# Optimization experiments

Measured on AMD Instinct MI355X. Metric: run time of the kernel, lower is better.

The kernel has to match this reference:

```python
import jax, jax.numpy as jnp
import numpy as np

ALPHA = 0.2  # LeakyReLU negative slope


def setup_inputs() -> dict:
    key = jax.random.key(0)
    k0, k1, k2, k3 = jax.random.split(key, 4)
    N, E, C_IN, H, C_PH = 50000, 800000, 128, 4, 32  # per-head dim = out_channels // num_heads
    node_feats = jax.random.normal(k0, (N, C_IN), dtype=jnp.float32)
    edge_index = jax.random.randint(k1, (2, E), 0, N, dtype=jnp.int64)
    # Linear(in_channels, num_heads * per_head): W is [H*C_PH, C_IN], b is [H*C_PH]
    W = jax.random.normal(k2, (H * C_PH, C_IN), dtype=jnp.float32) * 0.1
    b = jnp.zeros((H * C_PH,), dtype=jnp.float32)
    # attention vector a: [H, 2*C_PH]
    a = jax.random.normal(k3, (H, 2 * C_PH), dtype=jnp.float32) * 0.1
    return {"node_feats": node_feats, "edge_index": edge_index, "W": W, "b": b, "a": a}


def reference(node_feats, edge_index, W, b, a):
    H, twoC = a.shape
    C = twoC // 2
    N = node_feats.shape[0]
    # Linear projection, then split heads: [N, H, C]
    h = (node_feats @ W.T + b).reshape(N, H, C)
    # logits[e,h] = <h[src_e] ++ h[dst_e], a[h]> ; split the dot product so we
    # compute per-node partial scores once and gather scalars per edge.
    s_src = jnp.einsum('nhc,hc->nh', h, a[:, :C])   # [N, H]
    s_dst = jnp.einsum('nhc,hc->nh', h, a[:, C:])   # [N, H]
    logits = s_src[edge_index[0]] + s_dst[edge_index[1]]  # [E, H]
    logits = jax.nn.leaky_relu(logits, negative_slope=ALPHA)
    # Original applies softmax over dim=-2, i.e. across ALL edges per head.
    return jax.nn.softmax(logits, axis=0)
```

## Files before the change

### kernel.cpp

```cpp
#include <hip/hip_runtime.h>

#define ALPHA 0.2f

#define WS_BIAS 1024
#define WS_SUM  1032
#define WS_S    1040

__global__ void k_init(const float* __restrict__ W, const float* __restrict__ b,
                       const float* __restrict__ a, float* __restrict__ ws) {
    int t = threadIdx.x;
    #pragma unroll
    for (int h = 0; h < 4; ++h) {
        float accS = 0.f, accD = 0.f;
        #pragma unroll
        for (int c = 0; c < 32; ++c) {
            float wv = W[(h * 32 + c) * 128 + t];
            accS = fmaf(wv, a[h * 64 + c], accS);
            accD = fmaf(wv, a[h * 64 + 32 + c], accD);
        }
        ws[h * 128 + t] = accS;
        ws[512 + h * 128 + t] = accD;
    }
    if (t < 4) {
        float bs = 0.f, bd = 0.f;
        for (int c = 0; c < 32; ++c) {
            bs = fmaf(b[t * 32 + c], a[t * 64 + c], bs);
            bd = fmaf(b[t * 32 + c], a[t * 64 + 32 + c], bd);
        }
        ws[WS_BIAS + t] = bs;
        ws[WS_BIAS + 4 + t] = bd;
        ws[WS_SUM + t] = 0.f;
    }
}

__global__ __launch_bounds__(256) void k_proj(const float* __restrict__ x,
                                              float* __restrict__ ws, int N) {
    __shared__ float lw[1152];
    __shared__ float lb[8];
    int t = threadIdx.x;
    for (int idx = t; idx < 1024; idx += 256) {
        int k = idx & 127;
        int h = (idx >> 7) & 3;
        int base = (idx < 512) ? 0 : 576;
        lw[base + h * 144 + k + 4 * (k >> 5)] = ws[idx];
    }
    if (t < 8) lb[t] = ws[WS_BIAS + t];
    __syncthreads();

    int q = t & 3;
    int node = blockIdx.x * 64 + (t >> 2);
    float aS0=0,aS1=0,aS2=0,aS3=0,aD0=0,aD1=0,aD2=0,aD3=0;
    if (node < N) {
        const float4* xp = (const float4*)(x + (size_t)node * 128 + q * 32);
        int wb = q * 36;
        #pragma unroll
        for (int i = 0; i < 8; ++i) {
            float4 xv = xp[i];
            int o = wb + i * 4;
            float4 w;
            w = *(const float4*)&lw[o];          aS0 += xv.x*w.x + xv.y*w.y + xv.z*w.z + xv.w*w.w;
            w = *(const float4*)&lw[144 + o];    aS1 += xv.x*w.x + xv.y*w.y + xv.z*w.z + xv.w*w.w;
            w = *(const float4*)&lw[288 + o];    aS2 += xv.x*w.x + xv.y*w.y + xv.z*w.z + xv.w*w.w;
            w = *(const float4*)&lw[432 + o];    aS3 += xv.x*w.x + xv.y*w.y + xv.z*w.z + xv.w*w.w;
            w = *(const float4*)&lw[576 + o];    aD0 += xv.x*w.x + xv.y*w.y + xv.z*w.z + xv.w*w.w;
            w = *(const float4*)&lw[720 + o];    aD1 += xv.x*w.x + xv.y*w.y + xv.z*w.z + xv.w*w.w;
            w = *(const float4*)&lw[864 + o];    aD2 += xv.x*w.x + xv.y*w.y + xv.z*w.z + xv.w*w.w;
            w = *(const float4*)&lw[1008 + o];   aD3 += xv.x*w.x + xv.y*w.y + xv.z*w.z + xv.w*w.w;
        }
    }
    aS0 += __shfl_xor(aS0, 1); aS0 += __shfl_xor(aS0, 2);
    aS1 += __shfl_xor(aS1, 1); aS1 += __shfl_xor(aS1, 2);
    aS2 += __shfl_xor(aS2, 1); aS2 += __shfl_xor(aS2, 2);
    aS3 += __shfl_xor(aS3, 1); aS3 += __shfl_xor(aS3, 2);
    aD0 += __shfl_xor(aD0, 1); aD0 += __shfl_xor(aD0, 2);
    aD1 += __shfl_xor(aD1, 1); aD1 += __shfl_xor(aD1, 2);
    aD2 += __shfl_xor(aD2, 1); aD2 += __shfl_xor(aD2, 2);
    aD3 += __shfl_xor(aD3, 1); aD3 += __shfl_xor(aD3, 2);
    if (q == 0 && node < N) {
        float4* sp = (float4*)(ws + WS_S + (size_t)node * 8);
        sp[0] = make_float4(aS0 + lb[0], aS1 + lb[1], aS2 + lb[2], aS3 + lb[3]);
        sp[1] = make_float4(aD0 + lb[4], aD1 + lb[5], aD2 + lb[6], aD3 + lb[7]);
    }
}

__global__ __launch_bounds__(256) void k_edge(const int* __restrict__ ei,
                                              const float* __restrict__ s,
                                              float* __restrict__ out,
                                              float* __restrict__ sums, int E) {
    int tid = blockIdx.x * blockDim.x + threadIdx.x;
    int T = gridDim.x * blockDim.x;
    float l0 = 0.f, l1 = 0.f, l2 = 0.f, l3 = 0.f;
    for (int e = tid; e < E; e += T) {
        int src = ei[e];
        int dst = ei[E + e];
        float4 ss = *(const float4*)(s + (size_t)src * 8);
        float4 sd = *(const float4*)(s + (size_t)dst * 8 + 4);
        float z0 = ss.x + sd.x, z1 = ss.y + sd.y, z2 = ss.z + sd.z, z3 = ss.w + sd.w;
        z0 = (z0 >= 0.f) ? z0 : ALPHA * z0;
        z1 = (z1 >= 0.f) ? z1 : ALPHA * z1;
        z2 = (z2 >= 0.f) ? z2 : ALPHA * z2;
        z3 = (z3 >= 0.f) ? z3 : ALPHA * z3;
        float e0 = expf(z0), e1 = expf(z1), e2 = expf(z2), e3 = expf(z3);
        *(float4*)(out + (size_t)e * 4) = make_float4(e0, e1, e2, e3);
        l0 += e0; l1 += e1; l2 += e2; l3 += e3;
    }
    #pragma unroll
    for (int m = 1; m < 64; m <<= 1) {
        l0 += __shfl_xor(l0, m);
        l1 += __shfl_xor(l1, m);
        l2 += __shfl_xor(l2, m);
        l3 += __shfl_xor(l3, m);
    }
    __shared__ float red[4][4];
    int wv = threadIdx.x >> 6;
    if ((threadIdx.x & 63) == 0) {
        red[wv][0] = l0; red[wv][1] = l1; red[wv][2] = l2; red[wv][3] = l3;
    }
    __syncthreads();
    if (threadIdx.x < 4) {
        int h = threadIdx.x;
        atomicAdd(&sums[h], red[0][h] + red[1][h] + red[2][h] + red[3][h]);
    }
}

__global__ __launch_bounds__(256) void k_scale(float* __restrict__ out,
                                               const float* __restrict__ sums, int E) {
    __shared__ float inv[4];
    if (threadIdx.x < 4) inv[threadIdx.x] = 1.0f / sums[threadIdx.x];
    __syncthreads();
    int e = blockIdx.x * blockDim.x + threadIdx.x;
    if (e < E) {
        float4 v = *(const float4*)(out + (size_t)e * 4);
        v.x *= inv[0]; v.y *= inv[1]; v.z *= inv[2]; v.w *= inv[3];
        *(float4*)(out + (size_t)e * 4) = v;
    }
}

extern "C" void kernel_launch(void* const* d_in, const int* in_sizes, int n_in,
                              void* d_out, int out_size, void* d_ws, size_t ws_size,
                              hipStream_t stream) {
    const float* x  = (const float*)d_in[0];
    const int*   ei = (const int*)d_in[1];
    const float* W  = (const float*)d_in[2];
    const float* b  = (const float*)d_in[3];
    const float* a  = (const float*)d_in[4];
    float* out = (float*)d_out;
    float* ws  = (float*)d_ws;

    const int CIN = 128;
    int N = in_sizes[0] / CIN;
    int E = in_sizes[1] / 2;

    k_init<<<1, 128, 0, stream>>>(W, b, a, ws);
    k_proj<<<(N + 63) / 64, 256, 0, stream>>>(x, ws, N);
    k_edge<<<1024, 256, 0, stream>>>(ei, ws + WS_S, out, ws + WS_SUM, E);
    k_scale<<<(E + 255) / 256, 256, 0, stream>>>(out, ws + WS_SUM, E);
}
```

Measured before the change: 119.5 us.

## Fuse weight folding into projection and recompute edge exps instead of storing

```diff
diff --git a/kernel.cpp b/kernel.cpp
--- a/kernel.cpp
+++ b/kernel.cpp
@@ -2,49 +2,40 @@
 
 #define ALPHA 0.2f
 
-#define WS_BIAS 1024
-#define WS_SUM  1032
-#define WS_S    1040
-
-__global__ void k_init(const float* __restrict__ W, const float* __restrict__ b,
-                       const float* __restrict__ a, float* __restrict__ ws) {
-    int t = threadIdx.x;
-    #pragma unroll
-    for (int h = 0; h < 4; ++h) {
-        float accS = 0.f, accD = 0.f;
-        #pragma unroll
-        for (int c = 0; c < 32; ++c) {
-            float wv = W[(h * 32 + c) * 128 + t];
-            accS = fmaf(wv, a[h * 64 + c], accS);
-            accD = fmaf(wv, a[h * 64 + 32 + c], accD);
-        }
-        ws[h * 128 + t] = accS;
-        ws[512 + h * 128 + t] = accD;
-    }
-    if (t < 4) {
-        float bs = 0.f, bd = 0.f;
-        for (int c = 0; c < 32; ++c) {
-            bs = fmaf(b[t * 32 + c], a[t * 64 + c], bs);
-            bd = fmaf(b[t * 32 + c], a[t * 64 + 32 + c], bd);
-        }
-        ws[WS_BIAS + t] = bs;
-        ws[WS_BIAS + 4 + t] = bd;
-        ws[WS_SUM + t] = 0.f;
-    }
-}
+#define WS_SUM 0
+#define WS_S   64
 
 __global__ __launch_bounds__(256) void k_proj(const float* __restrict__ x,
+                                              const float* __restrict__ W,
+                                              const float* __restrict__ b,
+                                              const float* __restrict__ a,
                                               float* __restrict__ ws, int N) {
     __shared__ float lw[1152];
     __shared__ float lb[8];
     int t = threadIdx.x;
-    for (int idx = t; idx < 1024; idx += 256) {
+    #pragma unroll
+    for (int j = 0; j < 4; ++j) {
+        int idx = t + 256 * j;
         int k = idx & 127;
         int h = (idx >> 7) & 3;
-        int base = (idx < 512) ? 0 : 576;
-        lw[base + h * 144 + k + 4 * (k >> 5)] = ws[idx];
+        int dstf = idx >> 9;
+        const float* Wp = W + (size_t)(h * 32) * 128 + k;
+        const float* ap = a + h * 64 + dstf * 32;
+        float acc = 0.f;
+        #pragma unroll
+        for (int c = 0; c < 32; ++c)
+            acc = fmaf(Wp[(size_t)c * 128], ap[c], acc);
+        lw[dstf * 576 + h * 144 + k + 4 * (k >> 5)] = acc;
     }
-    if (t < 8) lb[t] = ws[WS_BIAS + t];
+    if (t < 8) {
+        int h = t & 3, dstf = t >> 2;
+        float acc = 0.f;
+        #pragma unroll
+        for (int c = 0; c < 32; ++c)
+            acc = fmaf(b[h * 32 + c], a[h * 64 + dstf * 32 + c], acc);
+        lb[t] = acc;
+    }
+    if (blockIdx.x == 0 && t < 4) ws[WS_SUM + t * 16] = 0.f;
     __syncthreads();
 
     int q = t & 3;
@@ -83,10 +74,14 @@
     }
 }
 
-__global__ __launch_bounds__(256) void k_edge(const int* __restrict__ ei,
-                                              const float* __restrict__ s,
-                                              float* __restrict__ out,
-                                              float* __restrict__ sums, int E) {
+__device__ __forceinline__ float leaky_exp(float z) {
+    z = (z >= 0.f) ? z : ALPHA * z;
+    return __expf(z);
+}
+
+__global__ __launch_bounds__(256) void k_edge_sum(const int* __restrict__ ei,
+                                                  const float* __restrict__ s,
+                                                  float* __restrict__ sums, int E) {
     int tid = blockIdx.x * blockDim.x + threadIdx.x;
     int T = gridDim.x * blockDim.x;
     float l0 = 0.f, l1 = 0.f, l2 = 0.f, l3 = 0.f;
@@ -95,14 +90,10 @@
         int dst = ei[E + e];
         float4 ss = *(const float4*)(s + (size_t)src * 8);
         float4 sd = *(const float4*)(s + (size_t)dst * 8 + 4);
-        float z0 = ss.x + sd.x, z1 = ss.y + sd.y, z2 = ss.z + sd.z, z3 = ss.w + sd.w;
-        z0 = (z0 >= 0.f) ? z0 : ALPHA * z0;
-        z1 = (z1 >= 0.f) ? z1 : ALPHA * z1;
-        z2 = (z2 >= 0.f) ? z2 : ALPHA * z2;
-        z3 = (z3 >= 0.f) ? z3 : ALPHA * z3;
-        float e0 = expf(z0), e1 = expf(z1), e2 = expf(z2), e3 = expf(z3);
-        *(float4*)(out + (size_t)e * 4) = make_float4(e0, e1, e2, e3);
-        l0 += e0; l1 += e1; l2 += e2; l3 += e3;
+        l0 += leaky_exp(ss.x + sd.x);
+        l1 += leaky_exp(ss.y + sd.y);
+        l2 += leaky_exp(ss.z + sd.z);
+        l3 += leaky_exp(ss.w + sd.w);
     }
     #pragma unroll
     for (int m = 1; m < 64; m <<= 1) {
@@ -119,19 +110,28 @@
     __syncthreads();
     if (threadIdx.x < 4) {
         int h = threadIdx.x;
-        atomicAdd(&sums[h], red[0][h] + red[1][h] + red[2][h] + red[3][h]);
+        atomicAdd(&sums[h * 16], red[0][h] + red[1][h] + red[2][h] + red[3][h]);
     }
 }
 
-__global__ __launch_bounds__(256) void k_scale(float* __restrict__ out,
-                                               const float* __restrict__ sums, int E) {
+__global__ __launch_bounds__(256) void k_finish(const int* __restrict__ ei,
+                                                const float* __restrict__ s,
+                                                const float* __restrict__ sums,
+                                                float* __restrict__ out, int E) {
     __shared__ float inv[4];
-    if (threadIdx.x < 4) inv[threadIdx.x] = 1.0f / sums[threadIdx.x];
+    if (threadIdx.x < 4) inv[threadIdx.x] = 1.0f / sums[threadIdx.x * 16];
     __syncthreads();
     int e = blockIdx.x * blockDim.x + threadIdx.x;
     if (e < E) {
-        float4 v = *(const float4*)(out + (size_t)e * 4);
-        v.x *= inv[0]; v.y *= inv[1]; v.z *= inv[2]; v.w *= inv[3];
+        int src = ei[e];
+        int dst = ei[E + e];
+        float4 ss = *(const float4*)(s + (size_t)src * 8);
+        float4 sd = *(const float4*)(s + (size_t)dst * 8 + 4);
+        float4 v;
+        v.x = leaky_exp(ss.x + sd.x) * inv[0];
+        v.y = leaky_exp(ss.y + sd.y) * inv[1];
+        v.z = leaky_exp(ss.z + sd.z) * inv[2];
+        v.w = leaky_exp(ss.w + sd.w) * inv[3];
         *(float4*)(out + (size_t)e * 4) = v;
     }
 }
@@ -151,8 +151,7 @@
     int N = in_sizes[0] / CIN;
     int E = in_sizes[1] / 2;
 
-    k_init<<<1, 128, 0, stream>>>(W, b, a, ws);
-    k_proj<<<(N + 63) / 64, 256, 0, stream>>>(x, ws, N);
-    k_edge<<<1024, 256, 0, stream>>>(ei, ws + WS_S, out, ws + WS_SUM, E);
-    k_scale<<<(E + 255) / 256, 256, 0, stream>>>(out, ws + WS_SUM, E);
+    k_proj<<<(N + 63) / 64, 256, 0, stream>>>(x, W, b, a, ws, N);
+    k_edge_sum<<<256, 256, 0, stream>>>(ei, ws + WS_S, ws + WS_SUM, E);
+    k_finish<<<(E + 255) / 256, 256, 0, stream>>>(ei, ws + WS_S, ws + WS_SUM, out, E);
 }
```

New measurement: 116.3 us. 2.6% less time.
